# Kernel optimization log

Measured on AMD Instinct MI355X. Metric: run time of the kernel, lower is better.

## Reference

```python
import jax, jax.numpy as jnp
import numpy as np

B, S, D, H = 4, 2048, 1024, 16
DH = D // H
LN_EPS = 1e-5


def setup_inputs() -> dict:
    key = jax.random.key(0)
    ks = jax.random.split(key, 12)
    scale = 0.02
    inp = {
        "x": jax.random.normal(ks[0], (B, S, D), dtype=jnp.float32),
        "attention_mask": jnp.ones((B, 1, 1, S), dtype=jnp.int32),
        # Linear weights stored torch-style: (out_features, in_features)
        "Wq": jax.random.normal(ks[1], (D, D), dtype=jnp.float32) * scale,
        "bq": jax.random.normal(ks[2], (D,), dtype=jnp.float32) * scale,
        "Wk": jax.random.normal(ks[3], (D, D), dtype=jnp.float32) * scale,
        "bk": jax.random.normal(ks[4], (D,), dtype=jnp.float32) * scale,
        "Wv": jax.random.normal(ks[5], (D, D), dtype=jnp.float32) * scale,
        "bv": jax.random.normal(ks[6], (D,), dtype=jnp.float32) * scale,
        "Wo": jax.random.normal(ks[7], (D, D), dtype=jnp.float32) * scale,
        "bo": jax.random.normal(ks[8], (D,), dtype=jnp.float32) * scale,
        "ln_w": jnp.ones((D,), dtype=jnp.float32),
        "ln_b": jnp.zeros((D,), dtype=jnp.float32),
    }
    return inp


def reference(x, attention_mask, Wq, bq, Wk, bk, Wv, bv, Wo, bo, ln_w, ln_b):
    b, s, d = x.shape
    # QKV projections (torch Linear: x @ W.T + b), split into heads -> [b, h, s, dh]
    def proj(W, bias):
        y = jnp.einsum('bsd,ed->bse', x, W) + bias
        return y.reshape(b, s, H, DH).transpose(0, 2, 1, 3)
    q = proj(Wq, bq)
    k = proj(Wk, bk)
    v = proj(Wv, bv)

    scores = jnp.einsum('bhqd,bhkd->bhqk', q, k) / jnp.sqrt(jnp.float32(DH))
    scores = jnp.where(attention_mask == 0, -jnp.inf, scores)
    # max-subtract softmax (stable), identical to jax.nn.softmax
    attn = jax.nn.softmax(scores, axis=-1)
    Hctx = jnp.einsum('bhqk,bhkd->bhqd', attn, v)  # [b, h, s, dh]
    Hctx = Hctx.transpose(0, 2, 1, 3).reshape(b, s, d)

    Hout = jnp.einsum('bsd,ed->bse', Hctx, Wo) + bo
    resid = x + Hout
    mu = jnp.mean(resid, axis=-1, keepdims=True)
    var = jnp.mean(jnp.square(resid - mu), axis=-1, keepdims=True)
    out = (resid - mu) / jnp.sqrt(var + LN_EPS) * ln_w + ln_b
    return out
```

## Files before the change

kernel.cpp:

```cpp
#include <hip/hip_runtime.h>
#include <hip/hip_bf16.h>
#include <stdint.h>

#define Bx  4
#define Sx  2048
#define Dx  1024
#define Hx  16
#define DHx 64
#define Mx  (Bx*Sx)

typedef short bf16x8 __attribute__((ext_vector_type(8)));
typedef float f32x4  __attribute__((ext_vector_type(4)));
typedef float f32x16 __attribute__((ext_vector_type(16)));

#define C1 0.18033688f

__device__ __forceinline__ unsigned short f2bf_u(float f) {
  union { float f; unsigned int u; } c; c.f = f;
  return (unsigned short)((c.u + 0x7fffu + ((c.u >> 16) & 1u)) >> 16);
}
__device__ __forceinline__ unsigned int pack2(float lo, float hi) {
  return ((unsigned int)f2bf_u(hi) << 16) | (unsigned int)f2bf_u(lo);
}
__device__ __forceinline__ unsigned int cvtpk(float lo_, float hi_) {
  unsigned int r;
  asm("v_cvt_pk_bf16_f32 %0, %1, %2" : "=v"(r) : "v"(lo_), "v"(hi_));
  return r;
}
__device__ __forceinline__ void swap32(unsigned int& d, unsigned int& s) {
  asm("v_permlane32_swap_b32 %0, %1" : "+v"(d), "+v"(s));
}

#define GLDS16(gp, lp) __builtin_amdgcn_global_load_lds( \
  (const __attribute__((address_space(1))) unsigned int*)(gp), \
  (__attribute__((address_space(3))) unsigned int*)(lp), 16, 0, 0)

__global__ __launch_bounds__(256) void prep_kernel(
    const float* __restrict__ x,  const float* __restrict__ Wq,
    const float* __restrict__ Wk, const float* __restrict__ Wv,
    const float* __restrict__ Wo, const int* __restrict__ mask,
    uint4* __restrict__ xb4, uint4* __restrict__ wb4,
    float* __restrict__ madd, unsigned* __restrict__ mb) {
  int bid = blockIdx.x, t = threadIdx.x;
  if (bid < 6144) {
    const float* src;
    uint4* dst;
    int i;
    if (bid < 4096) {
      src = x; dst = xb4; i = bid * 256 + t;
    } else {
      int wbid = bid - 4096;
      int widx = wbid >> 9;
      src = (widx == 0) ? Wq : (widx == 1) ? Wk : (widx == 2) ? Wv : Wo;
      dst = wb4 + (size_t)widx * 131072;
      i = (wbid & 511) * 256 + t;
    }
    const float4* s = (const float4*)src + (size_t)i * 2;
    float4 a = s[0], b = s[1];
    uint4 o;
    o.x = pack2(a.x, a.y); o.y = pack2(a.z, a.w);
    o.z = pack2(b.x, b.y); o.w = pack2(b.z, b.w);
    int ip = (i & ~3) | ((i & 3) ^ ((i >> 7) & 3) ^ ((i >> 9) & 3));
    dst[ip] = o;
  } else if (bid < 6176) {
    int i = (bid - 6144) * 256 + t;
    madd[i] = (mask[i] == 0) ? -1e30f : 0.0f;
  } else {
    int b = bid - 6176;
    if (t < 64) {
      int any = 0;
      if (t < 32) {
        for (int i = 0; i < 64; ++i) any |= (mask[b * Sx + t * 64 + i] == 0);
      }
      unsigned long long bits = __ballot(any != 0);
      if (t == 0) mb[b] = (unsigned)bits;
    }
  }
}

__global__ __launch_bounds__(256) void qkv_gemm(
    const short* __restrict__ xb, const short* __restrict__ wb,
    const float* __restrict__ bq, const float* __restrict__ bk,
    const float* __restrict__ bv,
    short* __restrict__ qb, short* __restrict__ kb, short* __restrict__ vb) {
  int lid = blockIdx.x + (blockIdx.y << 3) + (blockIdx.z << 9);
  int xcd = lid & 7;
  int idx = lid >> 3;
  int which = idx >> 6;
  int tt = idx & 63;
  int m0 = (xcd * 8 + (tt >> 3)) * 128;
  int n0 = (tt & 7) * 128;

  const short* Wm  = wb + (size_t)which * Dx * Dx;
  const float* bias = (which == 0) ? bq : (which == 1 ? bk : bv);

  __shared__ alignas(16) short smem[128 * 136];
  short* Al = smem;
  short* Bl = smem + 4096;

  int t = threadIdx.x;
  int l = t & 63, w = t >> 6;
  int wm = w >> 1, wn = w & 1;
  int srow = l >> 2;
  int scol = (l & 3) * 8;
  int fr = l & 15, fg = l >> 4;
  int pl = (fr & 3) ^ ((fr >> 2) & 3);
  int cA = ((fg ^ pl) << 3);

  f32x4 acc[4][4] = {};

  for (int k0 = 0; k0 < Dx; k0 += 32) {
#pragma unroll
    for (int i = 0; i < 2; ++i) {
      int r0 = (w * 2 + i) * 16;
      const short* ga = xb + (size_t)(m0 + r0 + srow) * Dx + k0 + scol;
      GLDS16(ga, &Al[r0 * 32]);
      const short* gb = Wm + (size_t)(n0 + r0 + srow) * Dx + k0 + scol;
      GLDS16(gb, &Bl[r0 * 32]);
    }
    __syncthreads();
    bf16x8 af[4], bfm[4];
#pragma unroll
    for (int i = 0; i < 4; ++i)
      af[i] = *(const bf16x8*)&Al[(wm * 64 + i * 16 + fr) * 32 + cA];
#pragma unroll
    for (int i = 0; i < 4; ++i)
      bfm[i] = *(const bf16x8*)&Bl[(wn * 64 + i * 16 + fr) * 32 + cA];
#pragma unroll
    for (int mi = 0; mi < 4; ++mi)
#pragma unroll
      for (int ni = 0; ni < 4; ++ni)
        acc[mi][ni] = __builtin_amdgcn_mfma_f32_16x16x32_bf16(
            af[mi], bfm[ni], acc[mi][ni], 0, 0, 0);
    __syncthreads();
  }

  if (which == 2) {
#pragma unroll
    for (int ni = 0; ni < 4; ++ni) {
      int n_l = wn * 64 + ni * 16 + fr;
      float bias_n = bias[n0 + n_l];
#pragma unroll
      for (int mi = 0; mi < 4; ++mi)
#pragma unroll
        for (int r = 0; r < 4; ++r) {
          int m_l = wm * 64 + mi * 16 + fg * 4 + r;
          smem[n_l * 136 + m_l] = (short)f2bf_u(acc[mi][ni][r] + bias_n);
        }
    }
    __syncthreads();
    int b = m0 >> 11, s0_ = m0 & 2047;
#pragma unroll
    for (int it = 0; it < 8; ++it) {
      int idx2 = t + it * 256;
      int n_l = idx2 >> 4, c = idx2 & 15;
      int4 v = *(const int4*)&smem[n_l * 136 + c * 8];
      int n = n0 + n_l, h = n >> 6, dh = n & 63;
      int chunk = (c & 7) ^ (dh & 7);
      size_t off = (size_t)(b * Hx + h) * Sx * 64
                 + (size_t)((s0_ >> 6) + (c >> 3)) * 4096
                 + dh * 64 + chunk * 8;
      *(int4*)&vb[off] = v;
    }
    return;
  }

#pragma unroll
  for (int ni = 0; ni < 4; ++ni) {
    int n = n0 + wn * 64 + ni * 16 + fr;
    int h = n >> 6, dh = n & 63;
    float bias_n = bias[n];
#pragma unroll
    for (int mi = 0; mi < 4; ++mi) {
#pragma unroll
      for (int r = 0; r < 4; ++r) {
        int m = m0 + wm * 64 + mi * 16 + fg * 4 + r;
        int b = m >> 11, s = m & 2047;
        float y = acc[mi][ni][r] + bias_n;
        size_t hb = (size_t)(b * Hx + h) * Sx * DHx;
        if (which == 0) {
          qb[hb + (size_t)s * DHx + dh] = (short)f2bf_u(y * C1);
        } else {
          kb[hb + (size_t)s * 64 + ((((dh >> 3) ^ (s & 7)) << 3) | (dh & 7))] =
              (short)f2bf_u(y);
        }
      }
    }
  }
}

__global__ __launch_bounds__(256, 2) void attn_kernel(
    const short* __restrict__ qb, const short* __restrict__ kb,
    const short* __restrict__ vb, const float* __restrict__ madd,
    const unsigned* __restrict__ maskbits, short* __restrict__ cbuf) {
  int bh = blockIdx.x;
  int qt = blockIdx.y;
  int b  = bh >> 4;

  __shared__ alignas(16) short Kl[2][4096];
  __shared__ alignas(16) short Vt[2][4096];

  int t = threadIdx.x, l = t & 63, w = t >> 6;
  int lo = l & 31, hi = l >> 5;

  const short* qgA = qb + ((size_t)bh * Sx + qt * 256 + w * 64 + lo) * 64;
  const short* qgB = qgA + 32 * 64;
  bf16x8 qfA[4], qfB[4];
#pragma unroll
  for (int ks = 0; ks < 4; ++ks) {
    qfA[ks] = *(const bf16x8*)&qgA[ks * 16 + hi * 8];
    qfB[ks] = *(const bf16x8*)&qgB[ks * 16 + hi * 8];
  }

  int koff[4], koff32[4];
#pragma unroll
  for (int ks = 0; ks < 4; ++ks) {
    int c = ((2 * ks + hi) ^ (lo & 7)) << 3;
    koff[ks]   = lo * 64 + c;
    koff32[ks] = (32 + lo) * 64 + c;
  }

  const short* kg = kb + (size_t)bh * Sx * 64;
  const short* vg = vb + (size_t)bh * Sx * 64;
  const float* mg = madd + b * Sx;
  unsigned mbits = maskbits[b];

  bf16x8 ones;
#pragma unroll
  for (int i = 0; i < 8; ++i) ones[i] = (short)0x3F80;

  f32x16 OA0 = {}, OA1 = {}, SsA = {};
  f32x16 OB0 = {}, OB1 = {}, SsB = {};

#define STAGE(tile, bf) do {                                              \
    const short* ks_ = kg + (size_t)(tile) * 4096;                        \
    const short* vs_ = vg + (size_t)(tile) * 4096;                        \
    GLDS16(ks_ + w * 512 + l * 8,        &Kl[bf][w * 512]);               \
    GLDS16(ks_ + 2048 + w * 512 + l * 8, &Kl[bf][2048 + w * 512]);        \
    GLDS16(vs_ + w * 512 + l * 8,        &Vt[bf][w * 512]);               \
    GLDS16(vs_ + 2048 + w * 512 + l * 8, &Vt[bf][2048 + w * 512]);        \
  } while (0)

#define TBODY(tile, cur) do {                                             \
    if ((tile) < 31) {                                                    \
      STAGE((tile) + 1, (cur) ^ 1);                                       \
      asm volatile("s_waitcnt vmcnt(4)" ::: "memory");                    \
    } else {                                                              \
      asm volatile("s_waitcnt vmcnt(0)" ::: "memory");                    \
    }                                                                     \
    __builtin_amdgcn_s_barrier();                                         \
    const short* Kb = &Kl[cur][0];                                        \
    const short* Vb = &Vt[cur][0];                                        \
    f32x16 sA0 = {}, sA1 = {}, sB0 = {}, sB1 = {};                        \
    __builtin_amdgcn_s_setprio(1);                                        \
    _Pragma("unroll")                                                     \
    for (int ks = 0; ks < 4; ++ks) {                                      \
      bf16x8 kf = *(const bf16x8*)&Kb[koff[ks]];                          \
      sA0 = __builtin_amdgcn_mfma_f32_32x32x16_bf16(kf, qfA[ks], sA0, 0, 0, 0); \
      sB0 = __builtin_amdgcn_mfma_f32_32x32x16_bf16(kf, qfB[ks], sB0, 0, 0, 0); \
    }                                                                     \
    _Pragma("unroll")                                                     \
    for (int ks = 0; ks < 4; ++ks) {                                      \
      bf16x8 kf = *(const bf16x8*)&Kb[koff32[ks]];                        \
      sA1 = __builtin_amdgcn_mfma_f32_32x32x16_bf16(kf, qfA[ks], sA1, 0, 0, 0); \
      sB1 = __builtin_amdgcn_mfma_f32_32x32x16_bf16(kf, qfB[ks], sB1, 0, 0, 0); \
    }                                                                     \
    __builtin_amdgcn_s_setprio(0);                                        \
    if ((mbits >> (tile)) & 1) {                                          \
      const float* mrow = mg + (tile) * 64;                               \
      _Pragma("unroll")                                                   \
      for (int r = 0; r < 16; ++r) {                                      \
        int key = (r & 3) + 8 * (r >> 2) + 4 * hi;                        \
        float m0_ = mrow[key], m1_ = mrow[32 + key];                      \
        sA0[r] += m0_; sA1[r] += m1_;                                     \
        sB0[r] += m0_; sB1[r] += m1_;                                     \
      }                                                                   \
    }                                                                     \
    _Pragma("unroll")                                                     \
    for (int r = 0; r < 16; ++r) {                                        \
      sA0[r] = __builtin_amdgcn_exp2f(sA0[r]);                            \
      sA1[r] = __builtin_amdgcn_exp2f(sA1[r]);                            \
      sB0[r] = __builtin_amdgcn_exp2f(sB0[r]);                            \
      sB1[r] = __builtin_amdgcn_exp2f(sB1[r]);                            \
    }                                                                     \
    __builtin_amdgcn_s_setprio(1);                                        \
    _Pragma("unroll")                                                     \
    for (int kbi = 0; kbi < 2; ++kbi) {                                   \
      _Pragma("unroll")                                                   \
      for (int half = 0; half < 2; ++half) {                              \
        int po = half * 8;                                                \
        unsigned int uA, uA2, vA, vA2, uB, uB2, vB, vB2;                  \
        if (kbi == 0) {                                                   \
          uA  = cvtpk(sA0[po + 0], sA0[po + 1]);                          \
          uA2 = cvtpk(sA0[po + 2], sA0[po + 3]);                          \
          vA  = cvtpk(sA0[po + 4], sA0[po + 5]);                          \
          vA2 = cvtpk(sA0[po + 6], sA0[po + 7]);                          \
          uB  = cvtpk(sB0[po + 0], sB0[po + 1]);                          \
          uB2 = cvtpk(sB0[po + 2], sB0[po + 3]);                          \
          vB  = cvtpk(sB0[po + 4], sB0[po + 5]);                          \
          vB2 = cvtpk(sB0[po + 6], sB0[po + 7]);                          \
        } else {                                                          \
          uA  = cvtpk(sA1[po + 0], sA1[po + 1]);                          \
          uA2 = cvtpk(sA1[po + 2], sA1[po + 3]);                          \
          vA  = cvtpk(sA1[po + 4], sA1[po + 5]);                          \
          vA2 = cvtpk(sA1[po + 6], sA1[po + 7]);                          \
          uB  = cvtpk(sB1[po + 0], sB1[po + 1]);                          \
          uB2 = cvtpk(sB1[po + 2], sB1[po + 3]);                          \
          vB  = cvtpk(sB1[po + 4], sB1[po + 5]);                          \
          vB2 = cvtpk(sB1[po + 6], sB1[po + 7]);                          \
        }                                                                 \
        swap32(vA, uA); swap32(vA2, uA2);                                 \
        swap32(vB, uB); swap32(vB2, uB2);                                 \
        union { unsigned int i[4]; bf16x8 v8; } puA, puB;                 \
        puA.i[0] = uA; puA.i[1] = uA2; puA.i[2] = vA; puA.i[3] = vA2;     \
        puB.i[0] = uB; puB.i[1] = uB2; puB.i[2] = vB; puB.i[3] = vB2;     \
        int vi = kbi * 2 + half;                                          \
        bf16x8 vf0 = *(const bf16x8*)&Vb[koff[vi]];                       \
        bf16x8 vf1 = *(const bf16x8*)&Vb[koff32[vi]];                     \
        OA0 = __builtin_amdgcn_mfma_f32_32x32x16_bf16(puA.v8, vf0, OA0, 0, 0, 0); \
        OA1 = __builtin_amdgcn_mfma_f32_32x32x16_bf16(puA.v8, vf1, OA1, 0, 0, 0); \
        SsA = __builtin_amdgcn_mfma_f32_32x32x16_bf16(puA.v8, ones, SsA, 0, 0, 0); \
        OB0 = __builtin_amdgcn_mfma_f32_32x32x16_bf16(puB.v8, vf0, OB0, 0, 0, 0); \
        OB1 = __builtin_amdgcn_mfma_f32_32x32x16_bf16(puB.v8, vf1, OB1, 0, 0, 0); \
        SsB = __builtin_amdgcn_mfma_f32_32x32x16_bf16(puB.v8, ones, SsB, 0, 0, 0); \
      }                                                                   \
    }                                                                     \
    __builtin_amdgcn_s_setprio(0);                                        \
    __builtin_amdgcn_s_barrier();                                        \
  } while (0)

  STAGE(0, 0);

  for (int tile = 0; tile < 32; tile += 2) {
    TBODY(tile, 0);
    TBODY(tile + 1, 1);
  }
#undef TBODY
#undef STAGE

  int h = bh & 15, bq_ = bh >> 4;
  int loLo = lo & 7, loCh = lo >> 3;
#pragma unroll
  for (int a = 0; a < 4; ++a) {
#pragma unroll
    for (int j = 0; j < 4; ++j) {
      int r = a * 4 + j;
      int srow = a * 8 + hi * 4 + j;
      int p = (srow & 3) ^ ((srow >> 2) & 3);
      int colp = ((loCh ^ p) << 3) | loLo;
      float linvA = __builtin_amdgcn_rcpf(SsA[r]);
      float linvB = __builtin_amdgcn_rcpf(SsB[r]);
      int sA = qt * 256 + w * 64 + srow;
      int sB = sA + 32;
      size_t rowbA = ((size_t)(bq_ * Sx + sA)) * Dx + h * 64;
      size_t rowbB = ((size_t)(bq_ * Sx + sB)) * Dx + h * 64;
      cbuf[rowbA + colp]      = (short)f2bf_u(OA0[r] * linvA);
      cbuf[rowbA + 32 + colp] = (short)f2bf_u(OA1[r] * linvA);
      cbuf[rowbB + colp]      = (short)f2bf_u(OB0[r] * linvB);
      cbuf[rowbB + 32 + colp] = (short)f2bf_u(OB1[r] * linvB);
    }
  }
}

__global__ __launch_bounds__(256) void proj_gemm(
    const short* __restrict__ cb, const short* __restrict__ wo,
    const float* __restrict__ bo, const float* __restrict__ x,
    float* __restrict__ out) {
  int lid = blockIdx.x + (blockIdx.y << 3);
  int xcd = lid & 7;
  int tt = lid >> 3;
  int m0 = (xcd * 8 + (tt >> 3)) * 128;
  int n0 = (tt & 7) * 128;

  __shared__ alignas(16) short Al[128 * 32];
  __shared__ alignas(16) short Bl[128 * 32];

  int t = threadIdx.x;
  int l = t & 63, w = t >> 6;
  int wm = w >> 1, wn = w & 1;
  int srow = l >> 2, scol = (l & 3) * 8;
  int fr = l & 15, fg = l >> 4;
  int pl = (fr & 3) ^ ((fr >> 2) & 3);
  int cA = ((fg ^ pl) << 3);

  f32x4 acc[4][4] = {};

  for (int k0 = 0; k0 < Dx; k0 += 32) {
#pragma unroll
    for (int i = 0; i < 2; ++i) {
      int r0 = (w * 2 + i) * 16;
      const short* ga = cb + (size_t)(m0 + r0 + srow) * Dx + k0 + scol;
      GLDS16(ga, &Al[r0 * 32]);
      const short* gb = wo + (size_t)(n0 + r0 + srow) * Dx + k0 + scol;
      GLDS16(gb, &Bl[r0 * 32]);
    }
    __syncthreads();
    bf16x8 af[4], bfm[4];
#pragma unroll
    for (int i = 0; i < 4; ++i)
      af[i] = *(const bf16x8*)&Al[(wm * 64 + i * 16 + fr) * 32 + cA];
#pragma unroll
    for (int i = 0; i < 4; ++i)
      bfm[i] = *(const bf16x8*)&Bl[(wn * 64 + i * 16 + fr) * 32 + cA];
#pragma unroll
    for (int mi = 0; mi < 4; ++mi)
#pragma unroll
      for (int ni = 0; ni < 4; ++ni)
        acc[mi][ni] = __builtin_amdgcn_mfma_f32_16x16x32_bf16(
            af[mi], bfm[ni], acc[mi][ni], 0, 0, 0);
    __syncthreads();
  }

#pragma unroll
  for (int ni = 0; ni < 4; ++ni) {
    int n = n0 + wn * 64 + ni * 16 + fr;
    float bias_n = bo[n];
#pragma unroll
    for (int mi = 0; mi < 4; ++mi) {
#pragma unroll
      for (int r = 0; r < 4; ++r) {
        int m = m0 + wm * 64 + mi * 16 + fg * 4 + r;
        float y = acc[mi][ni][r] + bias_n + x[(size_t)m * Dx + n];
        out[(size_t)m * Dx + n] = y;
      }
    }
  }
}

__global__ __launch_bounds__(256) void ln_kernel(float* __restrict__ io,
                                                 const float* __restrict__ lw,
                                                 const float* __restrict__ lb) {
  int row = blockIdx.x;
  float* p = io + (size_t)row * Dx;
  int c = threadIdx.x * 4;
  float4 v = *(float4*)&p[c];
  float s = v.x + v.y + v.z + v.w;
  float q = v.x * v.x + v.y * v.y + v.z * v.z + v.w * v.w;
#pragma unroll
  for (int d = 1; d < 64; d <<= 1) {
    s += __shfl_xor(s, d, 64);
    q += __shfl_xor(q, d, 64);
  }
  __shared__ float ss[4], qq[4];
  int l = threadIdx.x & 63, w = threadIdx.x >> 6;
  if (l == 0) { ss[w] = s; qq[w] = q; }
  __syncthreads();
  s = ss[0] + ss[1] + ss[2] + ss[3];
  q = qq[0] + qq[1] + qq[2] + qq[3];
  float mu = s * (1.f / Dx);
  float var = q * (1.f / Dx) - mu * mu;
  float rstd = rsqrtf(var + 1e-5f);
  float4 w4 = *(const float4*)&lw[c];
  float4 b4 = *(const float4*)&lb[c];
  float4 o;
  o.x = (v.x - mu) * rstd * w4.x + b4.x;
  o.y = (v.y - mu) * rstd * w4.y + b4.y;
  o.z = (v.z - mu) * rstd * w4.z + b4.z;
  o.w = (v.w - mu) * rstd * w4.w + b4.w;
  *(float4*)&p[c] = o;
}

extern "C" void kernel_launch(void* const* d_in, const int* in_sizes, int n_in,
                              void* d_out, int out_size, void* d_ws, size_t ws_size,
                              hipStream_t stream) {
  const float* x   = (const float*)d_in[0];
  const int*   msk = (const int*)d_in[1];
  const float* Wq  = (const float*)d_in[2];
  const float* bq  = (const float*)d_in[3];
  const float* Wk  = (const float*)d_in[4];
  const float* bk  = (const float*)d_in[5];
  const float* Wv  = (const float*)d_in[6];
  const float* bv  = (const float*)d_in[7];
  const float* Wo  = (const float*)d_in[8];
  const float* bo  = (const float*)d_in[9];
  const float* lnw = (const float*)d_in[10];
  const float* lnb = (const float*)d_in[11];
  float* out = (float*)d_out;

  char* ws = (char*)d_ws;
  short* xb = (short*)(ws);
  short* wb = (short*)(ws + (size_t)(16 << 20));
  short* qb = (short*)(ws + (size_t)(24 << 20));
  short* kb = (short*)(ws + (size_t)(40 << 20));
  short* vb = (short*)(ws + (size_t)(56 << 20));
  short* cb = (short*)(ws + (size_t)(72 << 20));
  float* madd = out;
  unsigned* mbits = (unsigned*)(out + Mx);

  prep_kernel<<<6180, 256, 0, stream>>>(x, Wq, Wk, Wv, Wo, msk,
                                        (uint4*)xb, (uint4*)wb, madd, mbits);
  qkv_gemm<<<dim3(8, 64, 3), 256, 0, stream>>>(xb, wb, bq, bk, bv, qb, kb, vb);
  attn_kernel<<<dim3(64, 8), 256, 0, stream>>>(qb, kb, vb, madd, mbits, cb);
  proj_gemm<<<dim3(8, 64), 256, 0, stream>>>(cb, wb + 3 * (size_t)(Dx * Dx), bo, x, out);
  ln_kernel<<<Mx, 256, 0, stream>>>(out, lnw, lnb);
}
```

Measured before the change: 206.4 us.

## Double-buffer QKV GEMM shared-memory tiles with async global-to-LDS prefetch

Splits the QKV projection GEMM's shared memory into two 8192-element buffers. The next K-step's global-to-LDS loads are issued before computing on the current buffer, with explicit vmcnt waits and raw s_barrier in place of __syncthreads. This is meant to hide global load latency behind MFMA work. It relies on hand-counted outstanding loads (vmcnt(4)), and the raw barriers may not order LDS accesses as strictly as __syncthreads does.

Measured after the change: 209.7 us. No clear change (+1.6%).

```diff
diff --git a/kernel.cpp b/kernel.cpp
--- a/kernel.cpp
+++ b/kernel.cpp
@@ -95,8 +95,6 @@
   const float* bias = (which == 0) ? bq : (which == 1 ? bk : bv);
 
   __shared__ alignas(16) short smem[128 * 136];
-  short* Al = smem;
-  short* Bl = smem + 4096;
 
   int t = threadIdx.x;
   int l = t & 63, w = t >> 6;
@@ -109,16 +107,32 @@
 
   f32x4 acc[4][4] = {};
 
-  for (int k0 = 0; k0 < Dx; k0 += 32) {
-#pragma unroll
-    for (int i = 0; i < 2; ++i) {
-      int r0 = (w * 2 + i) * 16;
-      const short* ga = xb + (size_t)(m0 + r0 + srow) * Dx + k0 + scol;
-      GLDS16(ga, &Al[r0 * 32]);
-      const short* gb = Wm + (size_t)(n0 + r0 + srow) * Dx + k0 + scol;
-      GLDS16(gb, &Bl[r0 * 32]);
-    }
-    __syncthreads();
+#define QSTAGE(step, bf) do {                                                  \
+    int kk = (step) * 32;                                                      \
+    _Pragma("unroll")                                                          \
+    for (int i = 0; i < 2; ++i) {                                              \
+      int r0 = (w * 2 + i) * 16;                                               \
+      GLDS16(xb + (size_t)(m0 + r0 + srow) * Dx + kk + scol,                   \
+             &smem[(bf) * 8192 + r0 * 32]);                                    \
+      GLDS16(Wm + (size_t)(n0 + r0 + srow) * Dx + kk + scol,                   \
+             &smem[(bf) * 8192 + 4096 + r0 * 32]);                             \
+    }                                                                          \
+  } while (0)
+
+  QSTAGE(0, 0);
+
+  for (int ks = 0; ks < 32; ++ks) {
+    int cur = ks & 1;
+    if (ks < 31) {
+      QSTAGE(ks + 1, cur ^ 1);
+      asm volatile("s_waitcnt vmcnt(4)" ::: "memory");
+    } else {
+      asm volatile("s_waitcnt vmcnt(0)" ::: "memory");
+    }
+    __builtin_amdgcn_s_barrier();
+
+    const short* Al = &smem[cur * 8192];
+    const short* Bl = &smem[cur * 8192 + 4096];
     bf16x8 af[4], bfm[4];
 #pragma unroll
     for (int i = 0; i < 4; ++i)
@@ -132,10 +146,12 @@
       for (int ni = 0; ni < 4; ++ni)
         acc[mi][ni] = __builtin_amdgcn_mfma_f32_16x16x32_bf16(
             af[mi], bfm[ni], acc[mi][ni], 0, 0, 0);
+    __builtin_amdgcn_s_barrier();
+  }
+#undef QSTAGE
+
+  if (which == 2) {
     __syncthreads();
-  }
-
-  if (which == 2) {
 #pragma unroll
     for (int ni = 0; ni < 4; ++ni) {
       int n_l = wn * 64 + ni * 16 + fr;
```

## Double-buffer QKV GEMM shared-memory tiles to overlap global loads with MFMA

Applied to the files above, without the earlier changes.

The QKV projection GEMM now splits its shared memory into two buffers. It prefetches the next k-step's A and B tiles while computing on the current ones, using explicit vmcnt waits and raw s_barrier in place of the two __syncthreads per iteration. Global pointers are hoisted out of the loop and the loop is unrolled by two. This aims to hide global-to-LDS load latency behind matrix work, relying on the existing 128x136 shared array being large enough for both buffers.

Result: faster. 202.1 us (-2.1%).

```diff
diff --git a/kernel.cpp b/kernel.cpp
--- a/kernel.cpp
+++ b/kernel.cpp
@@ -95,8 +95,6 @@
   const float* bias = (which == 0) ? bq : (which == 1 ? bk : bv);
 
   __shared__ alignas(16) short smem[128 * 136];
-  short* Al = smem;
-  short* Bl = smem + 4096;
 
   int t = threadIdx.x;
   int l = t & 63, w = t >> 6;
@@ -107,35 +105,60 @@
   int pl = (fr & 3) ^ ((fr >> 2) & 3);
   int cA = ((fg ^ pl) << 3);
 
+  int r0a = (w * 2 + 0) * 16;
+  int r0b = (w * 2 + 1) * 16;
+  const short* gA0 = xb + (size_t)(m0 + r0a + srow) * Dx + scol;
+  const short* gA1 = xb + (size_t)(m0 + r0b + srow) * Dx + scol;
+  const short* gB0 = Wm + (size_t)(n0 + r0a + srow) * Dx + scol;
+  const short* gB1 = Wm + (size_t)(n0 + r0b + srow) * Dx + scol;
+
   f32x4 acc[4][4] = {};
 
-  for (int k0 = 0; k0 < Dx; k0 += 32) {
-#pragma unroll
-    for (int i = 0; i < 2; ++i) {
-      int r0 = (w * 2 + i) * 16;
-      const short* ga = xb + (size_t)(m0 + r0 + srow) * Dx + k0 + scol;
-      GLDS16(ga, &Al[r0 * 32]);
-      const short* gb = Wm + (size_t)(n0 + r0 + srow) * Dx + k0 + scol;
-      GLDS16(gb, &Bl[r0 * 32]);
-    }
+#define QSTAGE(step, bf) do {                                             \
+    size_t ko = (size_t)(step) * 32;                                      \
+    GLDS16(gA0 + ko, &smem[(bf) * 8192 + r0a * 32]);                      \
+    GLDS16(gB0 + ko, &smem[(bf) * 8192 + 4096 + r0a * 32]);               \
+    GLDS16(gA1 + ko, &smem[(bf) * 8192 + r0b * 32]);                      \
+    GLDS16(gB1 + ko, &smem[(bf) * 8192 + 4096 + r0b * 32]);               \
+  } while (0)
+
+#define QBODY(step, cur) do {                                             \
+    if ((step) < 31) {                                                    \
+      QSTAGE((step) + 1, (cur) ^ 1);                                      \
+      asm volatile("s_waitcnt vmcnt(4)" ::: "memory");                    \
+    } else {                                                              \
+      asm volatile("s_waitcnt vmcnt(0)" ::: "memory");                    \
+    }                                                                     \
+    __builtin_amdgcn_s_barrier();                                         \
+    const short* Al = &smem[(cur) * 8192];                                \
+    const short* Bl = &smem[(cur) * 8192 + 4096];                         \
+    bf16x8 af[4], bfm[4];                                                 \
+    _Pragma("unroll")                                                     \
+    for (int i = 0; i < 4; ++i)                                           \
+      af[i] = *(const bf16x8*)&Al[(wm * 64 + i * 16 + fr) * 32 + cA];     \
+    _Pragma("unroll")                                                     \
+    for (int i = 0; i < 4; ++i)                                           \
+      bfm[i] = *(const bf16x8*)&Bl[(wn * 64 + i * 16 + fr) * 32 + cA];    \
+    _Pragma("unroll")                                                     \
+    for (int mi = 0; mi < 4; ++mi)                                        \
+      _Pragma("unroll")                                                   \
+      for (int ni = 0; ni < 4; ++ni)                                      \
+        acc[mi][ni] = __builtin_amdgcn_mfma_f32_16x16x32_bf16(            \
+            af[mi], bfm[ni], acc[mi][ni], 0, 0, 0);                       \
+    __builtin_amdgcn_s_barrier();                                         \
+  } while (0)
+
+  QSTAGE(0, 0);
+
+  for (int ks = 0; ks < 32; ks += 2) {
+    QBODY(ks, 0);
+    QBODY(ks + 1, 1);
+  }
+#undef QBODY
+#undef QSTAGE
+
+  if (which == 2) {
     __syncthreads();
-    bf16x8 af[4], bfm[4];
-#pragma unroll
-    for (int i = 0; i < 4; ++i)
-      af[i] = *(const bf16x8*)&Al[(wm * 64 + i * 16 + fr) * 32 + cA];
-#pragma unroll
-    for (int i = 0; i < 4; ++i)
-      bfm[i] = *(const bf16x8*)&Bl[(wn * 64 + i * 16 + fr) * 32 + cA];
-#pragma unroll
-    for (int mi = 0; mi < 4; ++mi)
-#pragma unroll
-      for (int ni = 0; ni < 4; ++ni)
-        acc[mi][ni] = __builtin_amdgcn_mfma_f32_16x16x32_bf16(
-            af[mi], bfm[ni], acc[mi][ni], 0, 0, 0);
-    __syncthreads();
-  }
-
-  if (which == 2) {
 #pragma unroll
     for (int ni = 0; ni < 4; ++ni) {
       int n_l = wn * 64 + ni * 16 + fr;
```
